# Kernel tuning notes

Hardware: AMD Instinct MI355X
Metric: run time of the kernel (lower is better)

## Reference

```python
import jax, jax.numpy as jnp
import numpy as np

TOKENS = 16384
HIDDEN = 4096
EXPERTS = 64


def setup_inputs() -> dict:
    key = jax.random.key(0)
    k1, k2, k3 = jax.random.split(key, 3)
    x = jax.random.normal(k1, (TOKENS, HIDDEN), dtype=jnp.float32)
    # int8-range quantized weights (stored as int32 per harness dtype set)
    weights_int8 = jax.random.randint(k2, (EXPERTS, HIDDEN), -128, 128, dtype=jnp.int32)
    # per-output-channel scales, small positive values
    scales = jax.random.uniform(k3, (EXPERTS,), dtype=jnp.float32, minval=1e-4, maxval=0.02)
    return {"x": x, "weights_int8": weights_int8, "scales": scales}


def reference(x, weights_int8, scales):
    # Dequantize: W[e, h] = int8_weight[e, h] * scale[e]   -> [EXPERTS, HIDDEN]
    w = weights_int8.astype(jnp.float32) * scales[:, None]
    w = w.astype(x.dtype)
    # F.linear(x, W) = x @ W^T  -> [..., EXPERTS]
    return jnp.einsum('th,eh->te', x, w)
```

## Files before the change

kernel.cpp:

```cpp
#include <hip/hip_runtime.h>
#include <hip/hip_bf16.h>

#define TOKENS 16384
#define HIDDEN 4096
#define EXPERTS 64

typedef __attribute__((ext_vector_type(8))) short short8;
typedef __attribute__((ext_vector_type(4))) float f32x4;

__device__ ushort g_B[128 * 4 * 64 * 8];

union Frag {
    uint4 u;
    short8 s;
};

__device__ __forceinline__ ushort f2bf_rtne(float f) {
    union { float f; unsigned u; } c; c.f = f;
    unsigned u = c.u;
    return (ushort)((u + 0x7FFF + ((u >> 16) & 1)) >> 16);
}

__device__ __forceinline__ unsigned pk_bf16(float lo, float hi) {
    __hip_bfloat162 h = __float22bfloat162_rn(make_float2(lo, hi));
    unsigned r;
    __builtin_memcpy(&r, &h, 4);
    return r;
}

__global__ __launch_bounds__(256) void prep_kernel(const int* __restrict__ w,
                                                   const float* __restrict__ sc,
                                                   float* __restrict__ out) {
    int tid = blockIdx.x * 256 + threadIdx.x;
    reinterpret_cast<float4*>(out)[tid] = make_float4(0.f, 0.f, 0.f, 0.f);

    int j    = tid & 7;
    int lane = (tid >> 3) & 63;
    int nt   = (tid >> 9) & 3;
    int kk   = tid >> 11;
    int e = nt * 16 + (lane & 15);
    int k = kk * 32 + (lane >> 4) * 8 + j;
    float v = (float)w[e * HIDDEN + k] * sc[e];
    g_B[tid] = f2bf_rtne(v);
}

__global__ __launch_bounds__(256, 4) void moe_router_kernel(const float* __restrict__ x,
                                                            float* __restrict__ out) {
    const int mb   = blockIdx.x;
    const int kq   = blockIdx.y;
    const int wave = threadIdx.x >> 6;
    const int lane = threadIdx.x & 63;

    const int row0 = mb * 64 + wave * 16;
    const int m    = row0 + (lane & 15);
    const int kb   = kq * 1024 + (lane >> 4) * 8;

    const float*  xp = x + (size_t)m * HIDDEN + kb;
    const ushort* bp = g_B + (size_t)kq * 65536 + lane * 8;

    f32x4 acc0 = {0.f, 0.f, 0.f, 0.f};
    f32x4 acc1 = {0.f, 0.f, 0.f, 0.f};
    f32x4 acc2 = {0.f, 0.f, 0.f, 0.f};
    f32x4 acc3 = {0.f, 0.f, 0.f, 0.f};

#pragma unroll 4
    for (int s = 0; s < 32; ++s) {
        float4 a0 = *reinterpret_cast<const float4*>(xp + s * 32);
        float4 a1 = *reinterpret_cast<const float4*>(xp + s * 32 + 4);
        Frag af;
        af.u.x = pk_bf16(a0.x, a0.y);
        af.u.y = pk_bf16(a0.z, a0.w);
        af.u.z = pk_bf16(a1.x, a1.y);
        af.u.w = pk_bf16(a1.z, a1.w);

        const uint4* bq = reinterpret_cast<const uint4*>(bp + (size_t)s * 2048);
        Frag b0, b1, b2, b3;
        b0.u = bq[0];
        b1.u = bq[64];
        b2.u = bq[128];
        b3.u = bq[192];

        acc0 = __builtin_amdgcn_mfma_f32_16x16x32_bf16(af.s, b0.s, acc0, 0, 0, 0);
        acc1 = __builtin_amdgcn_mfma_f32_16x16x32_bf16(af.s, b1.s, acc1, 0, 0, 0);
        acc2 = __builtin_amdgcn_mfma_f32_16x16x32_bf16(af.s, b2.s, acc2, 0, 0, 0);
        acc3 = __builtin_amdgcn_mfma_f32_16x16x32_bf16(af.s, b3.s, acc3, 0, 0, 0);
    }

    const int trow = row0 + (lane >> 4) * 4;
    const int col  = lane & 15;
    float* op = out + (size_t)trow * EXPERTS + col;
#pragma unroll
    for (int r = 0; r < 4; ++r) {
        atomicAdd(op + (size_t)r * EXPERTS + 0,  acc0[r]);
        atomicAdd(op + (size_t)r * EXPERTS + 16, acc1[r]);
        atomicAdd(op + (size_t)r * EXPERTS + 32, acc2[r]);
        atomicAdd(op + (size_t)r * EXPERTS + 48, acc3[r]);
    }
}

extern "C" void kernel_launch(void* const* d_in, const int* in_sizes, int n_in,
                              void* d_out, int out_size, void* d_ws, size_t ws_size,
                              hipStream_t stream) {
    const float* x  = (const float*)d_in[0];
    const int*   w  = (const int*)d_in[1];
    const float* sc = (const float*)d_in[2];
    float* out = (float*)d_out;

    prep_kernel<<<1024, 256, 0, stream>>>(w, sc, out);

    dim3 grid(TOKENS / 64, 4);
    moe_router_kernel<<<grid, 256, 0, stream>>>(x, out);
}
```

Measured before the change: 390.5 us.

## Replace split-K global atomics with in-block LDS reduction across 16 waves

Merges the four split-K blocks per 64-row tile into one 1024-thread block. Each group of four waves handles one K quarter and writes its partial sums to shared memory. After a barrier the four partials are summed and stored with plain vector writes. This removes the output zeroing in the prep kernel and the global float atomics. The cost is larger blocks with about 70 KB of LDS each, so fewer blocks fit per CU, and a block-wide barrier before the epilogue.

```diff
diff --git a/kernel.cpp b/kernel.cpp
--- a/kernel.cpp
+++ b/kernel.cpp
@@ -29,11 +29,8 @@
 }
 
 __global__ __launch_bounds__(256) void prep_kernel(const int* __restrict__ w,
-                                                   const float* __restrict__ sc,
-                                                   float* __restrict__ out) {
+                                                   const float* __restrict__ sc) {
     int tid = blockIdx.x * 256 + threadIdx.x;
-    reinterpret_cast<float4*>(out)[tid] = make_float4(0.f, 0.f, 0.f, 0.f);
-
     int j    = tid & 7;
     int lane = (tid >> 3) & 63;
     int nt   = (tid >> 9) & 3;
@@ -44,15 +41,18 @@
     g_B[tid] = f2bf_rtne(v);
 }
 
-__global__ __launch_bounds__(256, 4) void moe_router_kernel(const float* __restrict__ x,
-                                                            float* __restrict__ out) {
+__global__ __launch_bounds__(1024, 4) void moe_router_kernel(const float* __restrict__ x,
+                                                             float* __restrict__ out) {
+    __shared__ __align__(16) float lds[4][64][68];
+
     const int mb   = blockIdx.x;
-    const int kq   = blockIdx.y;
     const int wave = threadIdx.x >> 6;
     const int lane = threadIdx.x & 63;
+    const int rg   = wave & 3;
+    const int kq   = wave >> 2;
 
-    const int row0 = mb * 64 + wave * 16;
-    const int m    = row0 + (lane & 15);
+    const int rowl = rg * 16 + (lane & 15);
+    const int m    = mb * 64 + rowl;
     const int kb   = kq * 1024 + (lane >> 4) * 8;
 
     const float*  xp = x + (size_t)m * HIDDEN + kb;
@@ -86,16 +86,30 @@
         acc3 = __builtin_amdgcn_mfma_f32_16x16x32_bf16(af.s, b3.s, acc3, 0, 0, 0);
     }
 
-    const int trow = row0 + (lane >> 4) * 4;
+    const int lrow = rg * 16 + (lane >> 4) * 4;
     const int col  = lane & 15;
-    float* op = out + (size_t)trow * EXPERTS + col;
 #pragma unroll
     for (int r = 0; r < 4; ++r) {
-        atomicAdd(op + (size_t)r * EXPERTS + 0,  acc0[r]);
-        atomicAdd(op + (size_t)r * EXPERTS + 16, acc1[r]);
-        atomicAdd(op + (size_t)r * EXPERTS + 32, acc2[r]);
-        atomicAdd(op + (size_t)r * EXPERTS + 48, acc3[r]);
+        lds[kq][lrow + r][col +  0] = acc0[r];
+        lds[kq][lrow + r][col + 16] = acc1[r];
+        lds[kq][lrow + r][col + 32] = acc2[r];
+        lds[kq][lrow + r][col + 48] = acc3[r];
     }
+    __syncthreads();
+
+    const int t    = threadIdx.x;
+    const int rrow = t >> 4;
+    const int rcol = (t & 15) * 4;
+    float4 s0 = *reinterpret_cast<const float4*>(&lds[0][rrow][rcol]);
+    float4 s1 = *reinterpret_cast<const float4*>(&lds[1][rrow][rcol]);
+    float4 s2 = *reinterpret_cast<const float4*>(&lds[2][rrow][rcol]);
+    float4 s3 = *reinterpret_cast<const float4*>(&lds[3][rrow][rcol]);
+    float4 r4;
+    r4.x = (s0.x + s1.x) + (s2.x + s3.x);
+    r4.y = (s0.y + s1.y) + (s2.y + s3.y);
+    r4.z = (s0.z + s1.z) + (s2.z + s3.z);
+    r4.w = (s0.w + s1.w) + (s2.w + s3.w);
+    *reinterpret_cast<float4*>(out + ((size_t)mb * 64 + rrow) * EXPERTS + rcol) = r4;
 }
 
 extern "C" void kernel_launch(void* const* d_in, const int* in_sizes, int n_in,
@@ -106,8 +120,7 @@
     const float* sc = (const float*)d_in[2];
     float* out = (float*)d_out;
 
-    prep_kernel<<<1024, 256, 0, stream>>>(w, sc, out);
+    prep_kernel<<<1024, 256, 0, stream>>>(w, sc);
 
-    dim3 grid(TOKENS / 64, 4);
-    moe_router_kernel<<<grid, 256, 0, stream>>>(x, out);
+    moe_router_kernel<<<TOKENS / 64, 1024, 0, stream>>>(x, out);
 }
```

Result: no change. 383.7 us (-1.7%).

## Stage weight tiles in LDS and software-pipeline x loads with nontemporal hints

Applied to the files above, without the earlier changes.

Each block now copies its 64KB slice of the pre-packed bf16 weight fragments into shared memory and reads B from LDS instead of global memory. The K split doubles to 8 and blocks grow to 512 threads covering 128 rows. The main loop prefetches x two steps ahead and B one step ahead in registers, and uses nontemporal loads for x. This aims to hide global-load latency on the memory-bound x stream, at the cost of more atomics, an up-front LDS fill per block, and 64KB of LDS per block, which may reduce occupancy.

```diff
diff --git a/kernel.cpp b/kernel.cpp
--- a/kernel.cpp
+++ b/kernel.cpp
@@ -7,11 +7,12 @@
 
 typedef __attribute__((ext_vector_type(8))) short short8;
 typedef __attribute__((ext_vector_type(4))) float f32x4;
+typedef __attribute__((ext_vector_type(4))) unsigned int u32x4;
 
-__device__ ushort g_B[128 * 4 * 64 * 8];
+__device__ __align__(16) ushort g_B[128 * 4 * 64 * 8];
 
 union Frag {
-    uint4 u;
+    u32x4 u;
     short8 s;
 };
 
@@ -26,6 +27,11 @@
     unsigned r;
     __builtin_memcpy(&r, &h, 4);
     return r;
+}
+
+__device__ __forceinline__ void loadA(const float* p, f32x4& a0, f32x4& a1) {
+    a0 = __builtin_nontemporal_load(reinterpret_cast<const f32x4*>(p));
+    a1 = __builtin_nontemporal_load(reinterpret_cast<const f32x4*>(p) + 1);
 }
 
 __global__ __launch_bounds__(256) void prep_kernel(const int* __restrict__ w,
@@ -44,46 +50,67 @@
     g_B[tid] = f2bf_rtne(v);
 }
 
-__global__ __launch_bounds__(256, 4) void moe_router_kernel(const float* __restrict__ x,
+__global__ __launch_bounds__(512, 4) void moe_router_kernel(const float* __restrict__ x,
                                                             float* __restrict__ out) {
+    __shared__ u32x4 smB[4096];
+
     const int mb   = blockIdx.x;
     const int kq   = blockIdx.y;
-    const int wave = threadIdx.x >> 6;
-    const int lane = threadIdx.x & 63;
+    const int tid  = threadIdx.x;
+    const int wave = tid >> 6;
+    const int lane = tid & 63;
 
-    const int row0 = mb * 64 + wave * 16;
+    const u32x4* gB = reinterpret_cast<const u32x4*>(g_B) + (size_t)kq * 4096;
+#pragma unroll
+    for (int i = 0; i < 8; ++i) smB[tid + i * 512] = gB[tid + i * 512];
+    __syncthreads();
+
+    const int row0 = mb * 128 + wave * 16;
     const int m    = row0 + (lane & 15);
-    const int kb   = kq * 1024 + (lane >> 4) * 8;
-
-    const float*  xp = x + (size_t)m * HIDDEN + kb;
-    const ushort* bp = g_B + (size_t)kq * 65536 + lane * 8;
+    const int kb   = kq * 512 + (lane >> 4) * 8;
+    const float* xs = x + (size_t)m * HIDDEN + kb;
 
     f32x4 acc0 = {0.f, 0.f, 0.f, 0.f};
     f32x4 acc1 = {0.f, 0.f, 0.f, 0.f};
     f32x4 acc2 = {0.f, 0.f, 0.f, 0.f};
     f32x4 acc3 = {0.f, 0.f, 0.f, 0.f};
 
-#pragma unroll 4
-    for (int s = 0; s < 32; ++s) {
-        float4 a0 = *reinterpret_cast<const float4*>(xp + s * 32);
-        float4 a1 = *reinterpret_cast<const float4*>(xp + s * 32 + 4);
+    f32x4 a0c, a1c, a0n, a1n;
+    loadA(xs, a0c, a1c);
+    loadA(xs + 32, a0n, a1n);
+    u32x4 b0c = smB[lane];
+    u32x4 b1c = smB[lane + 64];
+    u32x4 b2c = smB[lane + 128];
+    u32x4 b3c = smB[lane + 192];
+
+    for (int s = 0; s < 16; ++s) {
+        f32x4 a0f = a0n, a1f = a1n;
+        if (s < 14) loadA(xs + (s + 2) * 32, a0f, a1f);
+
+        u32x4 b0n = b0c, b1n = b1c, b2n = b2c, b3n = b3c;
+        if (s < 15) {
+            const u32x4* bp = smB + (s + 1) * 256 + lane;
+            b0n = bp[0];
+            b1n = bp[64];
+            b2n = bp[128];
+            b3n = bp[192];
+        }
+
         Frag af;
-        af.u.x = pk_bf16(a0.x, a0.y);
-        af.u.y = pk_bf16(a0.z, a0.w);
-        af.u.z = pk_bf16(a1.x, a1.y);
-        af.u.w = pk_bf16(a1.z, a1.w);
+        af.u.x = pk_bf16(a0c.x, a0c.y);
+        af.u.y = pk_bf16(a0c.z, a0c.w);
+        af.u.z = pk_bf16(a1c.x, a1c.y);
+        af.u.w = pk_bf16(a1c.z, a1c.w);
 
-        const uint4* bq = reinterpret_cast<const uint4*>(bp + (size_t)s * 2048);
         Frag b0, b1, b2, b3;
-        b0.u = bq[0];
-        b1.u = bq[64];
-        b2.u = bq[128];
-        b3.u = bq[192];
-
+        b0.u = b0c; b1.u = b1c; b2.u = b2c; b3.u = b3c;
         acc0 = __builtin_amdgcn_mfma_f32_16x16x32_bf16(af.s, b0.s, acc0, 0, 0, 0);
         acc1 = __builtin_amdgcn_mfma_f32_16x16x32_bf16(af.s, b1.s, acc1, 0, 0, 0);
         acc2 = __builtin_amdgcn_mfma_f32_16x16x32_bf16(af.s, b2.s, acc2, 0, 0, 0);
         acc3 = __builtin_amdgcn_mfma_f32_16x16x32_bf16(af.s, b3.s, acc3, 0, 0, 0);
+
+        a0c = a0n; a1c = a1n; a0n = a0f; a1n = a1f;
+        b0c = b0n; b1c = b1n; b2c = b2n; b3c = b3n;
     }
 
     const int trow = row0 + (lane >> 4) * 4;
@@ -108,6 +135,6 @@
 
     prep_kernel<<<1024, 256, 0, stream>>>(w, sc, out);
 
-    dim3 grid(TOKENS / 64, 4);
-    moe_router_kernel<<<grid, 256, 0, stream>>>(x, out);
+    dim3 grid(TOKENS / 128, 8);
+    moe_router_kernel<<<grid, 512, 0, stream>>>(x, out);
 }
```

Result: faster. 352.6 us (-9.7%).
